# Kernel optimization log

Measured on AMD Instinct MI355X. Metric: run time of the kernel, lower is better.

The kernel has to match this reference:

```python
import jax, jax.numpy as jnp
import numpy as np

BLOCK_SIZE = 64
N_EMBD = 128
N_HEAD = 4
HEAD_DIM = N_EMBD // N_HEAD  # 32


def setup_inputs() -> dict:
    key = jax.random.key(0)
    kx, kq, kk, kv = jax.random.split(key, 4)
    B, T = 4096, 64
    x = jax.random.normal(kx, (B, T, N_EMBD), dtype=jnp.float32)
    # nn.Linear(n_embd, head_dim, bias=False): stored as [out,in] in torch,
    # here kept as [in, out] = [128, 32] so projection is x @ W.
    s = 1.0 / np.sqrt(N_EMBD)
    Wq = jax.random.uniform(kq, (N_EMBD, HEAD_DIM), jnp.float32, -s, s)
    Wk = jax.random.uniform(kk, (N_EMBD, HEAD_DIM), jnp.float32, -s, s)
    Wv = jax.random.uniform(kv, (N_EMBD, HEAD_DIM), jnp.float32, -s, s)
    return {"x": x, "Wq": Wq, "Wk": Wk, "Wv": Wv}


def reference(x, Wq, Wk, Wv):
    B, T, C = x.shape
    q = x @ Wq  # [B, T, Hd]
    k = x @ Wk
    v = x @ Wv
    scale = 1.0 / jnp.sqrt(jnp.asarray(k.shape[-1], x.dtype))
    wei = jnp.einsum("btd,bsd->bts", q, k) * scale  # [B, T, T]
    causal = jnp.tril(jnp.ones((T, T), dtype=bool))
    wei = jnp.where(causal, wei, -jnp.inf)
    wei = jax.nn.softmax(wei, axis=-1)
    out = jnp.einsum("bts,bsd->btd", wei, v)  # [B, T, Hd]
    return out
```

## Files before the change

kernel.cpp:

```cpp
#include <hip/hip_runtime.h>


#define TT 64
#define CC 128
#define HD 32

typedef __bf16 bf16_t;
typedef __bf16 bf8_t __attribute__((ext_vector_type(8)));
typedef __bf16 bf4_t __attribute__((ext_vector_type(4)));
typedef float  f4_t  __attribute__((ext_vector_type(4)));

__global__ __launch_bounds__(256) void prep_weights(
    const float* __restrict__ Wq, const float* __restrict__ Wk,
    const float* __restrict__ Wv, bf16_t* __restrict__ wf)
{
  int t = blockIdx.x * 256 + threadIdx.x;
  int j    = t & 7;
  int lane = (t >> 3) & 63;
  int kt   = (t >> 9) & 3;
  int n6   = t >> 11;
  int k    = kt * 32 + (lane >> 4) * 8 + j;
  int col  = (n6 & 1) * 16 + (lane & 15);
  const float* W = (n6 >> 1) == 0 ? Wq : ((n6 >> 1) == 1 ? Wk : Wv);
  float v = W[k * HD + col];
  if (n6 < 2) v *= 0.17677669529663687f;
  wf[t] = (bf16_t)v;
}

__global__ __launch_bounds__(64, 3) void head_fused(
    const float* __restrict__ x, const bf8_t* __restrict__ wf,
    float* __restrict__ out)
{
  __shared__ __align__(16) bf16_t ks[TT][40];
  __shared__ __align__(16) bf16_t vt[HD][72];
  __shared__ __align__(16) bf16_t ps[16][72];

  const int lane = threadIdx.x;
  const int quad = lane >> 4;
  const int l16  = lane & 15;
  const int b    = blockIdx.x;
  const float* __restrict__ xblk = x + (size_t)b * (TT * CC);
  float* __restrict__ ob = out + (size_t)b * (TT * HD);

  const f4_t zero4 = {0.f, 0.f, 0.f, 0.f};

  bf8_t wfr[24];
  bf8_t aq[4];
  float4 tf[4];

  auto load_half = [&](int i, int h) {
    #pragma unroll
    for (int u = 0; u < 2; ++u) {
      const float* s = xblk + (16 * i + l16) * CC + (2 * h + u) * 32 + quad * 8;
      tf[2 * u]     = *(const float4*)s;
      tf[2 * u + 1] = *(const float4*)(s + 4);
    }
  };
  auto cvt8 = [&](int u) -> bf8_t {
    float4 f0 = tf[2 * u], f1 = tf[2 * u + 1];
    bf8_t a;
    a[0] = (bf16_t)f0.x; a[1] = (bf16_t)f0.y; a[2] = (bf16_t)f0.z; a[3] = (bf16_t)f0.w;
    a[4] = (bf16_t)f1.x; a[5] = (bf16_t)f1.y; a[6] = (bf16_t)f1.z; a[7] = (bf16_t)f1.w;
    return a;
  };

  auto proj_tile = [&](int i) {
    f4_t acc[6];
    #pragma unroll
    for (int n = 0; n < 6; ++n) acc[n] = zero4;
    bf8_t a0 = cvt8(0), a1 = cvt8(1);
    load_half(i, 1);
    #pragma unroll
    for (int n = 0; n < 6; ++n)
      acc[n] = __builtin_amdgcn_mfma_f32_16x16x32_bf16(a0, wfr[n * 4 + 0], acc[n], 0, 0, 0);
    #pragma unroll
    for (int n = 0; n < 6; ++n)
      acc[n] = __builtin_amdgcn_mfma_f32_16x16x32_bf16(a1, wfr[n * 4 + 1], acc[n], 0, 0, 0);
    bf8_t a2 = cvt8(0), a3 = cvt8(1);
    if (i < 3) load_half(i + 1, 0);
    #pragma unroll
    for (int n = 0; n < 6; ++n)
      acc[n] = __builtin_amdgcn_mfma_f32_16x16x32_bf16(a2, wfr[n * 4 + 2], acc[n], 0, 0, 0);
    #pragma unroll
    for (int n = 0; n < 6; ++n)
      acc[n] = __builtin_amdgcn_mfma_f32_16x16x32_bf16(a3, wfr[n * 4 + 3], acc[n], 0, 0, 0);
    #pragma unroll
    for (int r = 0; r < 4; ++r) {
      int rl  = quad * 4 + r;
      int row = 16 * i + rl;
      ps[rl][l16]       = (bf16_t)acc[0][r];
      ps[rl][16 + l16]  = (bf16_t)acc[1][r];
      ks[row][l16]      = (bf16_t)acc[2][r];
      ks[row][16 + l16] = (bf16_t)acc[3][r];
    }
    bf4_t v0 = { (bf16_t)acc[4][0], (bf16_t)acc[4][1], (bf16_t)acc[4][2], (bf16_t)acc[4][3] };
    bf4_t v1 = { (bf16_t)acc[5][0], (bf16_t)acc[5][1], (bf16_t)acc[5][2], (bf16_t)acc[5][3] };
    *(bf4_t*)&vt[l16][16 * i + quad * 4]      = v0;
    *(bf4_t*)&vt[16 + l16][16 * i + quad * 4] = v1;
    aq[i] = *(const bf8_t*)&ps[l16][quad * 8];
  };

  bf8_t ones8;
  #pragma unroll
  for (int t = 0; t < 8; ++t) ones8[t] = (bf16_t)1.0f;

  auto sm_tile = [&](int i) {
    f4_t sc[4];
    bf8_t aqv = aq[i];
    #pragma unroll
    for (int j = 0; j < 4; ++j) {
      sc[j] = zero4;
      if (j <= i) {
        bf8_t bk = *(const bf8_t*)&ks[16 * j + l16][quad * 8];
        sc[j] = __builtin_amdgcn_mfma_f32_16x16x32_bf16(aqv, bk, zero4, 0, 0, 0);
      }
    }
    #pragma unroll
    for (int r = 0; r < 4; ++r) {
      int rl = quad * 4 + r;
      #pragma unroll
      for (int j = 0; j < 4; ++j) {
        if (j <= i) {
          bool valid = (j < i) | (l16 <= rl);
          float e = __expf(sc[j][r]);
          ps[rl][j * 16 + l16] = (bf16_t)(valid ? e : 0.f);
        } else if (j == (i | 1)) {
          ps[rl][j * 16 + l16] = (bf16_t)0.f;
        }
      }
    }
    f4_t o0 = zero4, o1 = zero4, osum = zero4;
    #pragma unroll
    for (int kk = 0; kk <= (i >> 1); ++kk) {
      int k0 = kk * 32 + quad * 8;
      bf8_t ap  = *(const bf8_t*)&ps[l16][k0];
      bf8_t bv0 = *(const bf8_t*)&vt[l16][k0];
      bf8_t bv1 = *(const bf8_t*)&vt[16 + l16][k0];
      o0   = __builtin_amdgcn_mfma_f32_16x16x32_bf16(ap, bv0, o0, 0, 0, 0);
      o1   = __builtin_amdgcn_mfma_f32_16x16x32_bf16(ap, bv1, o1, 0, 0, 0);
      osum = __builtin_amdgcn_mfma_f32_16x16x32_bf16(ap, ones8, osum, 0, 0, 0);
    }
    #pragma unroll
    for (int r = 0; r < 4; ++r) {
      int row = 16 * i + quad * 4 + r;
      float inv = __builtin_amdgcn_rcpf(osum[r]);
      ob[row * HD + l16]      = o0[r] * inv;
      ob[row * HD + 16 + l16] = o1[r] * inv;
    }
  };

  load_half(0, 0);
  #pragma unroll
  for (int t = 0; t < 24; ++t) wfr[t] = wf[t * 64 + lane];
  proj_tile(0);
  proj_tile(1);
  proj_tile(2);
  proj_tile(3);
  sm_tile(0);
  sm_tile(1);
  sm_tile(2);
  sm_tile(3);
}

extern "C" void kernel_launch(void* const* d_in, const int* in_sizes, int n_in,
                              void* d_out, int out_size, void* d_ws, size_t ws_size,
                              hipStream_t stream) {
  const float* x  = (const float*)d_in[0];
  const float* Wq = (const float*)d_in[1];
  const float* Wk = (const float*)d_in[2];
  const float* Wv = (const float*)d_in[3];
  float* out = (float*)d_out;
  bf16_t* wf = (bf16_t*)d_ws;
  int B = in_sizes[0] / (TT * CC);

  prep_weights<<<dim3(48), dim3(256), 0, stream>>>(Wq, Wk, Wv, wf);
  head_fused<<<dim3(B), dim3(64), 0, stream>>>(x, (const bf8_t*)wf, out);
}
```

Before: 231.7 us.

## Pack four batches per block, stage weights in LDS, keep K and V fragments in registers

Each block now runs four waves, one batch element per wave. The projection weights are staged once per block in shared memory instead of being held as 24 register fragments per lane. K fragments stay in registers, and V is handled in two 32-row halves with projection and softmax interleaved, which shrinks the per-wave LDS scratch. The aim is to cut register pressure and raise occupancy. The cost is extra LDS traffic for every weight fragment read and a block-wide barrier after the weight load.

```diff
diff --git a/kernel.cpp b/kernel.cpp
--- a/kernel.cpp
+++ b/kernel.cpp
@@ -27,26 +27,29 @@
   wf[t] = (bf16_t)v;
 }
 
-__global__ __launch_bounds__(64, 3) void head_fused(
-    const float* __restrict__ x, const bf8_t* __restrict__ wf,
+__global__ __launch_bounds__(256, 3) void head_fused(
+    const float* __restrict__ x, const float4* __restrict__ wf,
     float* __restrict__ out)
 {
-  __shared__ __align__(16) bf16_t ks[TT][40];
-  __shared__ __align__(16) bf16_t vt[HD][72];
-  __shared__ __align__(16) bf16_t ps[16][72];
-
-  const int lane = threadIdx.x;
+  __shared__ __align__(16) bf16_t wlds[12288];
+  __shared__ __align__(16) bf16_t qk[4][16][40];
+  __shared__ __align__(16) bf16_t pv[4][1280];
+
+  const int tid  = threadIdx.x;
+  const int wv   = tid >> 6;
+  const int lane = tid & 63;
   const int quad = lane >> 4;
   const int l16  = lane & 15;
-  const int b    = blockIdx.x;
-  const float* __restrict__ xblk = x + (size_t)b * (TT * CC);
-  float* __restrict__ ob = out + (size_t)b * (TT * HD);
+
+  const int e = blockIdx.x * 4 + wv;
+  const float* __restrict__ xblk = x + (size_t)e * (TT * CC);
+  float* __restrict__ ob = out + (size_t)e * (TT * HD);
 
   const f4_t zero4 = {0.f, 0.f, 0.f, 0.f};
 
-  bf8_t wfr[24];
-  bf8_t aq[4];
   float4 tf[4];
+  bf8_t kB[4];
+  bf8_t vLo[2], vHi[2];
 
   auto load_half = [&](int i, int h) {
     #pragma unroll
@@ -55,6 +58,21 @@
       tf[2 * u]     = *(const float4*)s;
       tf[2 * u + 1] = *(const float4*)(s + 4);
     }
+  };
+  load_half(0, 0);
+
+  #pragma unroll
+  for (int u = 0; u < 6; ++u) {
+    float4 w4 = wf[u * 256 + tid];
+    *(float4*)&wlds[(u * 256 + tid) * 8] = w4;
+  }
+  __syncthreads();
+
+  bf16_t (* __restrict__ qks)[40] = qk[wv];
+  bf16_t * __restrict__ pvb = pv[wv];
+
+  auto wfrag = [&](int t) -> bf8_t {
+    return *(const bf8_t*)&wlds[t * 512 + lane * 8];
   };
   auto cvt8 = [&](int u) -> bf8_t {
     float4 f0 = tf[2 * u], f1 = tf[2 * u + 1];
@@ -64,7 +82,7 @@
     return a;
   };
 
-  auto proj_tile = [&](int i) {
+  auto proj_tile = [&](int i, bf8_t& aqo) {
     f4_t acc[6];
     #pragma unroll
     for (int n = 0; n < 6; ++n) acc[n] = zero4;
@@ -72,48 +90,54 @@
     load_half(i, 1);
     #pragma unroll
     for (int n = 0; n < 6; ++n)
-      acc[n] = __builtin_amdgcn_mfma_f32_16x16x32_bf16(a0, wfr[n * 4 + 0], acc[n], 0, 0, 0);
-    #pragma unroll
-    for (int n = 0; n < 6; ++n)
-      acc[n] = __builtin_amdgcn_mfma_f32_16x16x32_bf16(a1, wfr[n * 4 + 1], acc[n], 0, 0, 0);
+      acc[n] = __builtin_amdgcn_mfma_f32_16x16x32_bf16(a0, wfrag(n * 4 + 0), acc[n], 0, 0, 0);
+    #pragma unroll
+    for (int n = 0; n < 6; ++n)
+      acc[n] = __builtin_amdgcn_mfma_f32_16x16x32_bf16(a1, wfrag(n * 4 + 1), acc[n], 0, 0, 0);
     bf8_t a2 = cvt8(0), a3 = cvt8(1);
     if (i < 3) load_half(i + 1, 0);
     #pragma unroll
     for (int n = 0; n < 6; ++n)
-      acc[n] = __builtin_amdgcn_mfma_f32_16x16x32_bf16(a2, wfr[n * 4 + 2], acc[n], 0, 0, 0);
-    #pragma unroll
-    for (int n = 0; n < 6; ++n)
-      acc[n] = __builtin_amdgcn_mfma_f32_16x16x32_bf16(a3, wfr[n * 4 + 3], acc[n], 0, 0, 0);
-    #pragma unroll
-    for (int r = 0; r < 4; ++r) {
-      int rl  = quad * 4 + r;
-      int row = 16 * i + rl;
-      ps[rl][l16]       = (bf16_t)acc[0][r];
-      ps[rl][16 + l16]  = (bf16_t)acc[1][r];
-      ks[row][l16]      = (bf16_t)acc[2][r];
-      ks[row][16 + l16] = (bf16_t)acc[3][r];
-    }
+      acc[n] = __builtin_amdgcn_mfma_f32_16x16x32_bf16(a2, wfrag(n * 4 + 2), acc[n], 0, 0, 0);
+    #pragma unroll
+    for (int n = 0; n < 6; ++n)
+      acc[n] = __builtin_amdgcn_mfma_f32_16x16x32_bf16(a3, wfrag(n * 4 + 3), acc[n], 0, 0, 0);
+    #pragma unroll
+    for (int r = 0; r < 4; ++r) {
+      int rl = quad * 4 + r;
+      qks[rl][l16]      = (bf16_t)acc[0][r];
+      qks[rl][16 + l16] = (bf16_t)acc[1][r];
+    }
+    aqo = *(const bf8_t*)&qks[l16][quad * 8];
+    #pragma unroll
+    for (int r = 0; r < 4; ++r) {
+      int rl = quad * 4 + r;
+      qks[rl][l16]      = (bf16_t)acc[2][r];
+      qks[rl][16 + l16] = (bf16_t)acc[3][r];
+    }
+    kB[i] = *(const bf8_t*)&qks[l16][quad * 8];
     bf4_t v0 = { (bf16_t)acc[4][0], (bf16_t)acc[4][1], (bf16_t)acc[4][2], (bf16_t)acc[4][3] };
     bf4_t v1 = { (bf16_t)acc[5][0], (bf16_t)acc[5][1], (bf16_t)acc[5][2], (bf16_t)acc[5][3] };
-    *(bf4_t*)&vt[l16][16 * i + quad * 4]      = v0;
-    *(bf4_t*)&vt[16 + l16][16 * i + quad * 4] = v1;
-    aq[i] = *(const bf8_t*)&ps[l16][quad * 8];
+    *(bf4_t*)&pvb[l16 * 40        + 16 * (i & 1) + quad * 4] = v0;
+    *(bf4_t*)&pvb[(16 + l16) * 40 + 16 * (i & 1) + quad * 4] = v1;
+  };
+
+  auto read_v = [&](int p) {
+    vLo[p] = *(const bf8_t*)&pvb[l16 * 40        + quad * 8];
+    vHi[p] = *(const bf8_t*)&pvb[(16 + l16) * 40 + quad * 8];
   };
 
   bf8_t ones8;
   #pragma unroll
   for (int t = 0; t < 8; ++t) ones8[t] = (bf16_t)1.0f;
 
-  auto sm_tile = [&](int i) {
+  auto sm_tile = [&](int i, bf8_t aqv) {
     f4_t sc[4];
-    bf8_t aqv = aq[i];
     #pragma unroll
     for (int j = 0; j < 4; ++j) {
       sc[j] = zero4;
-      if (j <= i) {
-        bf8_t bk = *(const bf8_t*)&ks[16 * j + l16][quad * 8];
-        sc[j] = __builtin_amdgcn_mfma_f32_16x16x32_bf16(aqv, bk, zero4, 0, 0, 0);
-      }
+      if (j <= i)
+        sc[j] = __builtin_amdgcn_mfma_f32_16x16x32_bf16(aqv, kB[j], zero4, 0, 0, 0);
     }
     #pragma unroll
     for (int r = 0; r < 4; ++r) {
@@ -122,23 +146,22 @@
       for (int j = 0; j < 4; ++j) {
         if (j <= i) {
           bool valid = (j < i) | (l16 <= rl);
-          float e = __expf(sc[j][r]);
-          ps[rl][j * 16 + l16] = (bf16_t)(valid ? e : 0.f);
+          float ev = __expf(sc[j][r]);
+          pvb[rl * 72 + j * 16 + l16] = (bf16_t)(valid ? ev : 0.f);
         } else if (j == (i | 1)) {
-          ps[rl][j * 16 + l16] = (bf16_t)0.f;
+          pvb[rl * 72 + j * 16 + l16] = (bf16_t)0.f;
         }
       }
     }
     f4_t o0 = zero4, o1 = zero4, osum = zero4;
     #pragma unroll
-    for (int kk = 0; kk <= (i >> 1); ++kk) {
-      int k0 = kk * 32 + quad * 8;
-      bf8_t ap  = *(const bf8_t*)&ps[l16][k0];
-      bf8_t bv0 = *(const bf8_t*)&vt[l16][k0];
-      bf8_t bv1 = *(const bf8_t*)&vt[16 + l16][k0];
-      o0   = __builtin_amdgcn_mfma_f32_16x16x32_bf16(ap, bv0, o0, 0, 0, 0);
-      o1   = __builtin_amdgcn_mfma_f32_16x16x32_bf16(ap, bv1, o1, 0, 0, 0);
-      osum = __builtin_amdgcn_mfma_f32_16x16x32_bf16(ap, ones8, osum, 0, 0, 0);
+    for (int kk = 0; kk < 2; ++kk) {
+      if (kk <= (i >> 1)) {
+        bf8_t ap = *(const bf8_t*)&pvb[l16 * 72 + kk * 32 + quad * 8];
+        o0   = __builtin_amdgcn_mfma_f32_16x16x32_bf16(ap, vLo[kk], o0, 0, 0, 0);
+        o1   = __builtin_amdgcn_mfma_f32_16x16x32_bf16(ap, vHi[kk], o1, 0, 0, 0);
+        osum = __builtin_amdgcn_mfma_f32_16x16x32_bf16(ap, ones8, osum, 0, 0, 0);
+      }
     }
     #pragma unroll
     for (int r = 0; r < 4; ++r) {
@@ -149,17 +172,17 @@
     }
   };
 
-  load_half(0, 0);
-  #pragma unroll
-  for (int t = 0; t < 24; ++t) wfr[t] = wf[t * 64 + lane];
-  proj_tile(0);
-  proj_tile(1);
-  proj_tile(2);
-  proj_tile(3);
-  sm_tile(0);
-  sm_tile(1);
-  sm_tile(2);
-  sm_tile(3);
+  bf8_t aq0, aq1;
+  proj_tile(0, aq0);
+  proj_tile(1, aq1);
+  read_v(0);
+  sm_tile(0, aq0);
+  sm_tile(1, aq1);
+  proj_tile(2, aq0);
+  proj_tile(3, aq1);
+  read_v(1);
+  sm_tile(2, aq0);
+  sm_tile(3, aq1);
 }
 
 extern "C" void kernel_launch(void* const* d_in, const int* in_sizes, int n_in,
@@ -174,5 +197,5 @@
   int B = in_sizes[0] / (TT * CC);
 
   prep_weights<<<dim3(48), dim3(256), 0, stream>>>(Wq, Wk, Wv, wf);
-  head_fused<<<dim3(B), dim3(64), 0, stream>>>(x, (const bf8_t*)wf, out);
+  head_fused<<<dim3(B / 4), dim3(256), 0, stream>>>(x, (const float4*)wf, out);
 }
```

Result: faster. 224.5 us (-3.1%).
